# Kernel tuning notes

Measured on AMD Instinct MI355X. Metric: run time of the kernel, lower is better.

## Reference

```python
import jax, jax.numpy as jnp
import numpy as np
import math

B, S, D, H, HD = 2, 2048, 2048, 16, 128
ROPE_THETA = 10000.0


def _rope_cache(seq_len, dim, base, dtype=jnp.float32):
    inv_freq = 1.0 / (base ** (jnp.arange(0, dim, 2, dtype=jnp.float32) / dim))
    t = jnp.arange(seq_len, dtype=jnp.float32)
    freqs = jnp.einsum('i,j->ij', t, inv_freq)          # [S, dim/2]
    emb = jnp.concatenate([freqs, freqs], axis=-1)       # [S, dim]
    return jnp.cos(emb).astype(dtype), jnp.sin(emb).astype(dtype)


def _rotate_half(x):
    x1, x2 = x[..., : x.shape[-1] // 2], x[..., x.shape[-1] // 2:]
    return jnp.concatenate([-x2, x1], axis=-1)


def setup_inputs() -> dict:
    key = jax.random.key(0)
    ks = jax.random.split(key, 6)
    hidden_states = jax.random.normal(ks[0], (B, S, D), dtype=jnp.float32) * 0.02
    w_scale = 1.0 / math.sqrt(D)
    Wq = jax.random.normal(ks[1], (D, D), dtype=jnp.float32) * w_scale
    Wk = jax.random.normal(ks[2], (D, D), dtype=jnp.float32) * w_scale
    Wv = jax.random.normal(ks[3], (D, D), dtype=jnp.float32) * w_scale
    Wo = jax.random.normal(ks[4], (D, D), dtype=jnp.float32) * w_scale
    # additive causal mask [B, 1, S, S]: 0 on/below diag, large negative above
    causal = jnp.tril(jnp.ones((S, S), dtype=bool))
    attention_mask = jnp.where(causal, 0.0, -1e9).astype(jnp.float32)
    attention_mask = jnp.broadcast_to(attention_mask[None, None], (B, 1, S, S))
    position_ids = jnp.broadcast_to(jnp.arange(S, dtype=jnp.int32)[None], (B, S))
    return {
        'hidden_states': hidden_states,
        'attention_mask': attention_mask,
        'position_ids': position_ids,
        'Wq': Wq, 'Wk': Wk, 'Wv': Wv, 'Wo': Wo,
    }


def reference(hidden_states, attention_mask, position_ids, Wq, Wk, Wv, Wo):
    bsz, q_len, _ = hidden_states.shape
    # projections (torch Linear: x @ W.T), then split heads -> [B, H, S, HD]
    def proj(W):
        return jnp.einsum('bsd,ed->bse', hidden_states, W).reshape(bsz, q_len, H, HD).transpose(0, 2, 1, 3)
    q, k, v = proj(Wq), proj(Wk), proj(Wv)
    cos_c, sin_c = _rope_cache(q_len, HD, ROPE_THETA, hidden_states.dtype)
    cos = cos_c[position_ids][:, None]  # [B, 1, S, HD]
    sin = sin_c[position_ids][:, None]
    q = q * cos + _rotate_half(q) * sin
    k = k * cos + _rotate_half(k) * sin
    scores = jnp.einsum('bhqd,bhkd->bhqk', q, k) / math.sqrt(HD)
    scores = scores + attention_mask
    attn_weights = jax.nn.softmax(scores.astype(jnp.float32), axis=-1).astype(q.dtype)
    attn_out = jnp.einsum('bhqk,bhkd->bhqd', attn_weights, v)
    attn_out = attn_out.transpose(0, 2, 1, 3).reshape(bsz, q_len, D)
    out = jnp.einsum('bsd,ed->bse', attn_out, Wo)
    return out
```

## Files before the change

kernel.cpp:

```cpp
#include <hip/hip_runtime.h>

typedef __bf16 bf16;
typedef __bf16 bf16x8 __attribute__((ext_vector_type(8)));
typedef float f32x4 __attribute__((ext_vector_type(4)));

#define D_MODEL 2048
#define SEQ 2048
#define NH 16
#define HEAD_DIM 128
#define NBATCH 2
#define SM_SCALE 0.08838834764831845f
#define WSEG 4194304
#define NT_TILES 32

typedef __attribute__((address_space(1))) const void* gas_cp;
typedef __attribute__((address_space(3))) void* las_p;
__device__ __forceinline__ void ll16(const bf16* g, bf16* l) {
  __builtin_amdgcn_global_load_lds((gas_cp)g, (las_p)l, 16, 0, 0);
}

__device__ __forceinline__ bf16x8 cvt8(const float* p) {
  float4 a = *(const float4*)p;
  float4 b = *(const float4*)(p + 4);
  bf16x8 v;
  v[0] = (bf16)a.x; v[1] = (bf16)a.y; v[2] = (bf16)a.z; v[3] = (bf16)a.w;
  v[4] = (bf16)b.x; v[5] = (bf16)b.y; v[6] = (bf16)b.z; v[7] = (bf16)b.w;
  return v;
}

__global__ __launch_bounds__(256)
void cvt_hidden(const float* __restrict__ src, bf16* __restrict__ dst) {
  size_t i = ((size_t)blockIdx.x * 256 + threadIdx.x) * 8;
  *(bf16x8*)(dst + i) = cvt8(src + i);
}

__global__ __launch_bounds__(256)
void cvt_weights(const float* __restrict__ w0, const float* __restrict__ w1,
                 const float* __restrict__ w2, const float* __restrict__ w3,
                 bf16* __restrict__ dst) {
  const float* src = (blockIdx.y == 0) ? w0 : (blockIdx.y == 1) ? w1
                   : (blockIdx.y == 2) ? w2 : w3;
  size_t i = ((size_t)blockIdx.x * 256 + threadIdx.x) * 8;
  *(bf16x8*)(dst + (size_t)blockIdx.y * WSEG + i) = cvt8(src + i);
}

#define LDF256(DA, DB, SB, KX)                                               \
  _Pragma("unroll") for (int mi = 0; mi < 8; mi++)                           \
      DA[mi] = *(const bf16x8*)((SB) + ((arowQ + mi * 16) << 7) + (KX));     \
  DB[0] = *(const bf16x8*)((SB) + 32768 + (qb0 << 7) + (KX));                \
  DB[1] = *(const bf16x8*)((SB) + 32768 + (qb1 << 7) + (KX));                \
  DB[2] = *(const bf16x8*)((SB) + 32768 + (qb2 << 7) + (KX));                \
  DB[3] = *(const bf16x8*)((SB) + 32768 + (qb3 << 7) + (KX));

#define MM256(AF, BF)                                                        \
  _Pragma("unroll") for (int mi = 0; mi < 8; mi++)                           \
  _Pragma("unroll") for (int ni = 0; ni < 4; ni++)                           \
      acc[mi][ni] = __builtin_amdgcn_mfma_f32_16x16x32_bf16(                 \
          AF[mi], BF[ni], acc[mi][ni], 0, 0, 0);

#define ST2(GP, ROW0, KT, LB)                                                \
  ll16((GP) + (size_t)((ROW0) + w * 8 + l8) * D_MODEL + (KT) * 64 + kelem,   \
       (bf16*)((LB) + w * 1024));

__global__ __launch_bounds__(512, 2)
void gemm256(const bf16* __restrict__ A, const bf16* __restrict__ W,
             bf16* __restrict__ Qo, bf16* __restrict__ Ko,
             bf16* __restrict__ Vo, const int* __restrict__ pos_ids) {
  __shared__ __align__(16) char smem[131072];

  const int tid  = threadIdx.x;
  const int lane = tid & 63;
  const int w    = tid >> 6;
  const int quad = lane >> 4, l15 = lane & 15;
  const int l8   = lane >> 3, l7 = lane & 7;
  const int kelem = 8 * (l7 ^ l8);
  const int wm2 = w >> 2;
  const int wn2 = w & 3;
  const int hh  = wn2 >> 1;
  const int cb  = (wn2 & 1) * 32;

  const int bid = blockIdx.x;
  const int lin = (bid & 7) * 48 + (bid >> 3);
  const int by = lin / 24, bx = lin % 24;
  const int mBase = by << 8, nBase = bx << 8;

  const int kx0 = (quad * 16) ^ ((l15 & 7) << 4);
  const int kx1 = kx0 ^ 64;
  const int arowQ = wm2 * 128 + l15;
  const int qb0 = hh * 128 + cb + l15;
  const int qb1 = qb0 + 16, qb2 = qb0 + 64, qb3 = qb0 + 80;

  f32x4 acc[8][4];
#pragma unroll
  for (int i = 0; i < 8; i++)
#pragma unroll
    for (int j = 0; j < 4; j++) acc[i][j] = 0.0f;

  bf16x8 aP[8], bP[4];
  bf16x8 aQ[8], bQ[4];

  {
    char* s0 = smem;
    ST2(A, mBase,       0, s0 + 0);
    ST2(A, mBase + 64,  0, s0 + 8192);
    ST2(A, mBase + 128, 0, s0 + 16384);
    ST2(A, mBase + 192, 0, s0 + 24576);
    ST2(W, nBase,       0, s0 + 32768);
    ST2(W, nBase + 64,  0, s0 + 40960);
    ST2(W, nBase + 128, 0, s0 + 49152);
    ST2(W, nBase + 192, 0, s0 + 57344);
  }
  asm volatile("s_waitcnt vmcnt(0)" ::: "memory");
  __builtin_amdgcn_s_barrier();
  LDF256(aP, bP, smem, kx0);

  int buf = 0;
  for (int t = 0; t < NT_TILES; ++t) {
    char* const Sb = smem + buf * 65536;
    char* const Ob = smem + (buf ^ 1) * 65536;
    const bool pf  = (t + 1 < NT_TILES);

    LDF256(aQ, bQ, Sb, kx1);
    if (pf) {
      ST2(A, mBase,       t + 1, Ob + 0);
      ST2(A, mBase + 64,  t + 1, Ob + 8192);
      ST2(A, mBase + 128, t + 1, Ob + 16384);
      ST2(A, mBase + 192, t + 1, Ob + 24576);
      ST2(W, nBase,       t + 1, Ob + 32768);
      ST2(W, nBase + 64,  t + 1, Ob + 40960);
      ST2(W, nBase + 128, t + 1, Ob + 49152);
      ST2(W, nBase + 192, t + 1, Ob + 57344);
    }
    __builtin_amdgcn_sched_barrier(0);
    __builtin_amdgcn_s_setprio(1);
    MM256(aP, bP);
    __builtin_amdgcn_s_setprio(0);
    asm volatile("s_waitcnt lgkmcnt(0)" ::: "memory");
    asm volatile("s_waitcnt vmcnt(0)" ::: "memory");
    __builtin_amdgcn_s_barrier();

    if (pf) {
      LDF256(aP, bP, Ob, kx0);
    }
    __builtin_amdgcn_sched_barrier(0);
    __builtin_amdgcn_s_setprio(1);
    MM256(aQ, bQ);
    __builtin_amdgcn_s_setprio(0);
    asm volatile("s_waitcnt lgkmcnt(0)" ::: "memory");

    buf ^= 1;
  }

  const int matrix = nBase >> 11;
  const int nb     = nBase & 2047;
  if (matrix == 2) {
    const int h = (nb >> 7) + hh;
#pragma unroll
    for (int mi = 0; mi < 8; mi++)
#pragma unroll
      for (int ni = 0; ni < 4; ni++) {
        const int hd = cb + (ni & 1) * 16 + (ni >> 1) * 64 + l15;
#pragma unroll
        for (int r = 0; r < 4; r++) {
          int m = mBase + wm2 * 128 + mi * 16 + quad * 4 + r;
          int b = m >> 11, s2 = m & 2047;
          Vo[((size_t)((b * NH + h) * HEAD_DIM + hd)) * SEQ + s2] =
              (bf16)acc[mi][ni][r];
        }
      }
  } else {
    bf16* Out = (matrix == 0) ? Qo : Ko;
    float invf[2];
#pragma unroll
    for (int ni = 0; ni < 2; ni++)
      invf[ni] = __expf(-(float)(cb + ni * 16 + l15) *
                        (9.210340371976184f / 64.0f));
#pragma unroll
    for (int mi = 0; mi < 8; mi++)
#pragma unroll
      for (int r = 0; r < 4; r++) {
        int m = mBase + wm2 * 128 + mi * 16 + quad * 4 + r;
        float pos = (float)pos_ids[m];
        bf16* op = Out + (size_t)m * D_MODEL + nb + hh * 128 + cb + l15;
#pragma unroll
        for (int ni = 0; ni < 2; ni++) {
          float sn, cs;
          __sincosf(pos * invf[ni], &sn, &cs);
          float q0 = acc[mi][ni][r];
          float q1 = acc[mi][ni + 2][r];
          op[ni * 16]      = (bf16)(q0 * cs - q1 * sn);
          op[ni * 16 + 64] = (bf16)(q1 * cs + q0 * sn);
        }
      }
  }
}

#define LDFRAG(DA, DB, SB, KX)                                               \
  _Pragma("unroll") for (int mi = 0; mi < 4; mi++)                           \
      DA[mi] = *(const bf16x8*)((SB) + ((arow + mi * 16) << 7) + (KX));      \
  DB[0] = *(const bf16x8*)((SB) + 16384 + (rb0 << 7) + (KX));                \
  DB[1] = *(const bf16x8*)((SB) + 16384 + (rb1 << 7) + (KX));                \
  DB[2] = *(const bf16x8*)((SB) + 16384 + (rb2 << 7) + (KX));                \
  DB[3] = *(const bf16x8*)((SB) + 16384 + (rb3 << 7) + (KX));

#define MMAC(AF, BF)                                                         \
  _Pragma("unroll") for (int mi = 0; mi < 4; mi++)                           \
  _Pragma("unroll") for (int ni = 0; ni < 4; ni++)                           \
      acc[mi][ni] = __builtin_amdgcn_mfma_f32_16x16x32_bf16(                 \
          AF[mi], BF[ni], acc[mi][ni], 0, 0, 0);

#define ST1(GP, ROW0, KT, LB)                                                \
  ll16((GP) + (size_t)((ROW0) + w * 8 + l8) * D_MODEL + (KT) * 64 + kelem,   \
       (bf16*)((LB) + w * 1024));

__global__ __launch_bounds__(512, 2)
void gemm_proj(const bf16* __restrict__ A, const bf16* __restrict__ W,
               float* __restrict__ C) {
  __shared__ __align__(16) char smem[147456];

  const int tid  = threadIdx.x;
  const int lane = tid & 63;
  const int w    = tid >> 6;
  const int quad = lane >> 4, l15 = lane & 15;
  const int l8   = lane >> 3, l7 = lane & 7;
  const int kelem = 8 * (l7 ^ l8);
  const int wm = w >> 2;
  const int wn = w & 3;

  const int bid = blockIdx.x;
  const int lin = (bid & 7) * 32 + (bid >> 3);
  const int by = lin >> 3, bx = lin & 7;
  const int mBase = by << 7, nBase = bx << 8;

  const int kx0 = (quad * 16) ^ ((l15 & 7) << 4);
  const int kx1 = kx0 ^ 64;
  const int arow = wm * 64 + l15;
  const int rb0 = wn * 64 + l15;
  const int rb1 = rb0 + 16, rb2 = rb0 + 32, rb3 = rb0 + 48;

  f32x4 acc[4][4];
#pragma unroll
  for (int i = 0; i < 4; i++)
#pragma unroll
    for (int j = 0; j < 4; j++) acc[i][j] = 0.0f;

  bf16x8 aP[4], bP[4], aQ[4], bQ[4];

  {
    char* s0 = smem;
    char* s1 = smem + 49152;
    ST1(A, mBase,       0, s0 + 0);
    ST1(A, mBase + 64,  0, s0 + 8192);
    ST1(W, nBase,       0, s0 + 16384);
    ST1(W, nBase + 64,  0, s0 + 24576);
    ST1(W, nBase + 128, 0, s0 + 32768);
    ST1(W, nBase + 192, 0, s0 + 40960);
    ST1(A, mBase,       1, s1 + 0);
    ST1(A, mBase + 64,  1, s1 + 8192);
    ST1(W, nBase,       1, s1 + 16384);
    ST1(W, nBase + 64,  1, s1 + 24576);
    ST1(W, nBase + 128, 1, s1 + 32768);
    ST1(W, nBase + 192, 1, s1 + 40960);
  }
  asm volatile("s_waitcnt vmcnt(6)" ::: "memory");
  __builtin_amdgcn_s_barrier();
  LDFRAG(aP, bP, smem, kx0);

  int buf = 0;
  for (int t = 0; t < NT_TILES; ++t) {
    char* const Sb  = smem + buf * 49152;
    const int  nb1  = (buf + 1 == 3) ? 0 : buf + 1;
    const int  pb   = (buf + 2 >= 3) ? buf - 1 : buf + 2;
    char* const Nb  = smem + nb1 * 49152;
    char* const Pb  = smem + pb * 49152;
    const bool pf   = (t + 2 < NT_TILES);

    LDFRAG(aQ, bQ, Sb, kx1);
    if (pf) {
      ST1(A, mBase,      t + 2, Pb + 0);
      ST1(A, mBase + 64, t + 2, Pb + 8192);
      ST1(W, nBase,      t + 2, Pb + 16384);
    }
    __builtin_amdgcn_sched_barrier(0);
    __builtin_amdgcn_s_setprio(1);
    MMAC(aP, bP);
    __builtin_amdgcn_s_setprio(0);
    asm volatile("s_waitcnt lgkmcnt(0)" ::: "memory");
    if (pf)
      asm volatile("s_waitcnt vmcnt(3)" ::: "memory");
    else
      asm volatile("s_waitcnt vmcnt(0)" ::: "memory");
    __builtin_amdgcn_s_barrier();

    if (t + 1 < NT_TILES) {
      LDFRAG(aP, bP, Nb, kx0);
    }
    if (pf) {
      ST1(W, nBase + 64,  t + 2, Pb + 24576);
      ST1(W, nBase + 128, t + 2, Pb + 32768);
      ST1(W, nBase + 192, t + 2, Pb + 40960);
    }
    __builtin_amdgcn_sched_barrier(0);
    __builtin_amdgcn_s_setprio(1);
    MMAC(aQ, bQ);
    __builtin_amdgcn_s_setprio(0);
    asm volatile("s_waitcnt lgkmcnt(0)" ::: "memory");
    __builtin_amdgcn_s_barrier();

    buf = nb1;
  }

#pragma unroll
  for (int mi = 0; mi < 4; mi++) {
    const int m = mBase + wm * 64 + mi * 16 + quad * 4;
#pragma unroll
    for (int ni = 0; ni < 4; ni++) {
      const int n = nBase + wn * 64 + ni * 16 + l15;
      float* cp = C + (size_t)m * D_MODEL + n;
#pragma unroll
      for (int r = 0; r < 4; r++) cp[(size_t)r * D_MODEL] = acc[mi][ni][r];
    }
  }
}

__global__ __launch_bounds__(256, 3)
void attn_mfma(const bf16* __restrict__ Q, const bf16* __restrict__ K,
               const bf16* __restrict__ Vt, bf16* __restrict__ O) {
  __shared__ __align__(16) bf16 K_lds[64 * 136];
  __shared__ __align__(16) bf16 V_lds[128 * 72];
  __shared__ __align__(16) bf16 P_lds[64 * 72];

  const int tid  = threadIdx.x;
  const int lane = tid & 63;
  const int w    = tid >> 6;
  const int quad = lane >> 4, l15 = lane & 15;
  const int s    = 31 - blockIdx.y;
  const int bh   = blockIdx.x;
  const size_t qkBase = (size_t)(bh >> 4) * SEQ * D_MODEL + (size_t)(bh & 15) * HEAD_DIM;
  const size_t vBase  = (size_t)bh * HEAD_DIM * SEQ;

  const int qbase = s * 64 + w * 16;

  bf16x8 qa[4];
#pragma unroll
  for (int kk = 0; kk < 4; kk++)
    qa[kk] = *(const bf16x8*)(Q + qkBase + (size_t)(qbase + l15) * D_MODEL + kk * 32 + quad * 8);

  bf16x8 ones;
#pragma unroll
  for (int i = 0; i < 8; i++) ones[i] = (bf16)1.0f;

  f32x4 oacc[8], ls;
#pragma unroll
  for (int ni = 0; ni < 8; ni++) oacc[ni] = 0.0f;
  ls = 0.0f;

  const int ntiles = s + 1;

  bf16x8 kr[4], vr[4];
  auto loadKV = [&](int t0) {
#pragma unroll
    for (int i = 0; i < 4; i++) {
      int c = tid + 256 * i;
      kr[i] = *(const bf16x8*)(K + qkBase + (size_t)(t0 + (c >> 4)) * D_MODEL + (c & 15) * 8);
    }
#pragma unroll
    for (int i = 0; i < 4; i++) {
      int c = tid + 256 * i;
      vr[i] = *(const bf16x8*)(Vt + vBase + (size_t)(c >> 3) * SEQ + t0 + (c & 7) * 8);
    }
  };
  loadKV(0);

  const int prow = w * 16;

  for (int tt = 0; tt < ntiles; tt++) {
    const int t0 = tt * 64;
    __syncthreads();
#pragma unroll
    for (int i = 0; i < 4; i++) {
      int c = tid + 256 * i;
      *(bf16x8*)&K_lds[(c >> 4) * 136 + (c & 15) * 8] = kr[i];
    }
#pragma unroll
    for (int i = 0; i < 4; i++) {
      int c = tid + 256 * i;
      *(bf16x8*)&V_lds[(c >> 3) * 72 + (c & 7) * 8] = vr[i];
    }
    __syncthreads();
    if (tt + 1 < ntiles) loadKV(t0 + 64);

    f32x4 sacc[4];
#pragma unroll
    for (int ni = 0; ni < 4; ni++) sacc[ni] = 0.0f;
#pragma unroll
    for (int kk = 0; kk < 4; kk++) {
#pragma unroll
      for (int ni = 0; ni < 4; ni++) {
        bf16x8 kf = *(const bf16x8*)&K_lds[(ni * 16 + l15) * 136 + kk * 32 + quad * 8];
        sacc[ni] = __builtin_amdgcn_mfma_f32_16x16x32_bf16(qa[kk], kf, sacc[ni], 0, 0, 0);
      }
    }

    if (tt == s) {
#pragma unroll
      for (int r = 0; r < 4; r++) {
        int qrow = qbase + quad * 4 + r;
#pragma unroll
        for (int ni = 0; ni < 4; ni++) {
          int tcol = t0 + ni * 16 + l15;
          float pv = (tcol <= qrow) ? __expf(fminf(sacc[ni][r] * SM_SCALE, 30.0f)) : 0.0f;
          P_lds[(prow + quad * 4 + r) * 72 + ni * 16 + l15] = (bf16)pv;
        }
      }
    } else {
#pragma unroll
      for (int r = 0; r < 4; r++)
#pragma unroll
        for (int ni = 0; ni < 4; ni++)
          P_lds[(prow + quad * 4 + r) * 72 + ni * 16 + l15] =
              (bf16)__expf(fminf(sacc[ni][r] * SM_SCALE, 30.0f));
    }

#pragma unroll
    for (int kk2 = 0; kk2 < 2; kk2++) {
      bf16x8 pf = *(const bf16x8*)&P_lds[(prow + l15) * 72 + kk2 * 32 + quad * 8];
#pragma unroll
      for (int ni = 0; ni < 8; ni++) {
        bf16x8 vf = *(const bf16x8*)&V_lds[(ni * 16 + l15) * 72 + kk2 * 32 + quad * 8];
        oacc[ni] = __builtin_amdgcn_mfma_f32_16x16x32_bf16(pf, vf, oacc[ni], 0, 0, 0);
      }
      ls = __builtin_amdgcn_mfma_f32_16x16x32_bf16(pf, ones, ls, 0, 0, 0);
    }
  }

#pragma unroll
  for (int r = 0; r < 4; r++) {
    float inv = 1.0f / ls[r];
    bf16* op = O + qkBase + (size_t)(qbase + quad * 4 + r) * D_MODEL;
#pragma unroll
    for (int ni = 0; ni < 8; ni++)
      op[ni * 16 + l15] = (bf16)(oacc[ni][r] * inv);
  }
}

extern "C" void kernel_launch(void* const* d_in, const int* in_sizes, int n_in,
                              void* d_out, int out_size, void* d_ws, size_t ws_size,
                              hipStream_t stream) {
  const float* hidden = (const float*)d_in[0];
  const int* pos = (const int*)d_in[2];
  const float* Wq = (const float*)d_in[3];
  const float* Wk = (const float*)d_in[4];
  const float* Wv = (const float*)d_in[5];
  const float* Wo = (const float*)d_in[6];
  float* out = (float*)d_out;

  const size_t TENS = (size_t)NBATCH * SEQ * D_MODEL;
  bf16* Qb = (bf16*)d_ws;
  bf16* Kb = Qb + TENS;
  bf16* Vt = Kb + TENS;
  bf16* AO = Vt + TENS;
  bf16* Hb = AO + TENS;
  bf16* Wb = Hb + TENS;

  cvt_hidden<<<dim3(TENS / 2048), dim3(256), 0, stream>>>(hidden, Hb);
  cvt_weights<<<dim3(WSEG / 2048, 4), dim3(256), 0, stream>>>(Wq, Wk, Wv, Wo, Wb);

  gemm256<<<dim3(384), dim3(512), 0, stream>>>(Hb, Wb, Qb, Kb, Vt, pos);

  attn_mfma<<<dim3(NBATCH * NH, 32), dim3(256), 0, stream>>>(Qb, Kb, Vt, AO);

  gemm_proj<<<dim3(256), dim3(512), 0, stream>>>(
      AO, Wb + 3 * (size_t)WSEG, out);
}
```

Baseline: 370.4 us.

## Rewrite attention with 128-row Q blocks, async LDS double-buffered KV, swizzled layout

The attention kernel now processes 128 query rows per block with 8 waves, so each K/V tile loaded into LDS is reused by twice as many queries. K/V tiles are copied straight into double-buffered LDS with global_load_lds instead of passing through registers, and an XOR swizzle replaces row padding to avoid bank conflicts. Waves whose rows lie entirely before the current key tile skip the tile's compute, which keeps the causal work balanced. In exchange there is a full vmcnt wait and barrier every tile, and fewer blocks with more LDS per block, which lowers occupancy.

```diff
diff --git a/kernel.cpp b/kernel.cpp
--- a/kernel.cpp
+++ b/kernel.cpp
@@ -323,28 +323,31 @@
   }
 }
 
-__global__ __launch_bounds__(256, 3)
-void attn_mfma(const bf16* __restrict__ Q, const bf16* __restrict__ K,
-               const bf16* __restrict__ Vt, bf16* __restrict__ O) {
-  __shared__ __align__(16) bf16 K_lds[64 * 136];
-  __shared__ __align__(16) bf16 V_lds[128 * 72];
-  __shared__ __align__(16) bf16 P_lds[64 * 72];
+__global__ __launch_bounds__(512, 2)
+void attn_v2(const bf16* __restrict__ Q, const bf16* __restrict__ K,
+             const bf16* __restrict__ Vt, bf16* __restrict__ O) {
+  __shared__ __align__(16) bf16 Kl[2][64 * 128];
+  __shared__ __align__(16) bf16 Vl[2][128 * 64];
+  __shared__ __align__(16) bf16 P_lds[128 * 72];
 
   const int tid  = threadIdx.x;
   const int lane = tid & 63;
   const int w    = tid >> 6;
   const int quad = lane >> 4, l15 = lane & 15;
-  const int s    = 31 - blockIdx.y;
+  const int l8   = lane >> 3, l7 = lane & 7;
+  const int qi   = 15 - (int)blockIdx.y;
   const int bh   = blockIdx.x;
   const size_t qkBase = (size_t)(bh >> 4) * SEQ * D_MODEL + (size_t)(bh & 15) * HEAD_DIM;
   const size_t vBase  = (size_t)bh * HEAD_DIM * SEQ;
 
-  const int qbase = s * 64 + w * 16;
+  const int qbw  = qi * 128 + w * 16;
+  const int prow = w * 16;
+  const int kswz = (l15 & 7) << 3;
 
   bf16x8 qa[4];
 #pragma unroll
   for (int kk = 0; kk < 4; kk++)
-    qa[kk] = *(const bf16x8*)(Q + qkBase + (size_t)(qbase + l15) * D_MODEL + kk * 32 + quad * 8);
+    qa[kk] = *(const bf16x8*)(Q + qkBase + (size_t)(qbw + l15) * D_MODEL + kk * 32 + quad * 8);
 
   bf16x8 ones;
 #pragma unroll
@@ -355,89 +358,87 @@
   for (int ni = 0; ni < 8; ni++) oacc[ni] = 0.0f;
   ls = 0.0f;
 
-  const int ntiles = s + 1;
-
-  bf16x8 kr[4], vr[4];
-  auto loadKV = [&](int t0) {
-#pragma unroll
-    for (int i = 0; i < 4; i++) {
-      int c = tid + 256 * i;
-      kr[i] = *(const bf16x8*)(K + qkBase + (size_t)(t0 + (c >> 4)) * D_MODEL + (c & 15) * 8);
-    }
-#pragma unroll
-    for (int i = 0; i < 4; i++) {
-      int c = tid + 256 * i;
-      vr[i] = *(const bf16x8*)(Vt + vBase + (size_t)(c >> 3) * SEQ + t0 + (c & 7) * 8);
-    }
-  };
-  loadKV(0);
-
-  const int prow = w * 16;
-
-  for (int tt = 0; tt < ntiles; tt++) {
+  const int nt = 2 * qi + 2;
+
+#define STAGE_KV(T0, BUF)                                                    \
+  _Pragma("unroll") for (int i_ = 0; i_ < 2; i_++) {                         \
+    const int u_ = w * 2 + i_;                                               \
+    const int rK = u_ * 4 + quad;                                            \
+    ll16(K + qkBase + (size_t)((T0) + rK) * D_MODEL + 8 * (l15 ^ (rK & 7)),  \
+         &Kl[BUF][u_ * 512]);                                                \
+    const int rV = u_ * 8 + l8;                                              \
+    ll16(Vt + vBase + (size_t)rV * SEQ + (T0) + 8 * (l7 ^ (rV & 7)),         \
+         &Vl[BUF][u_ * 512]);                                                \
+  }
+
+  STAGE_KV(0, 0);
+  asm volatile("s_waitcnt vmcnt(0)" ::: "memory");
+  __builtin_amdgcn_s_barrier();
+
+  int cur = 0;
+  for (int tt = 0; tt < nt; ++tt, cur ^= 1) {
     const int t0 = tt * 64;
-    __syncthreads();
-#pragma unroll
-    for (int i = 0; i < 4; i++) {
-      int c = tid + 256 * i;
-      *(bf16x8*)&K_lds[(c >> 4) * 136 + (c & 15) * 8] = kr[i];
-    }
-#pragma unroll
-    for (int i = 0; i < 4; i++) {
-      int c = tid + 256 * i;
-      *(bf16x8*)&V_lds[(c >> 3) * 72 + (c & 7) * 8] = vr[i];
-    }
-    __syncthreads();
-    if (tt + 1 < ntiles) loadKV(t0 + 64);
-
-    f32x4 sacc[4];
-#pragma unroll
-    for (int ni = 0; ni < 4; ni++) sacc[ni] = 0.0f;
-#pragma unroll
-    for (int kk = 0; kk < 4; kk++) {
-#pragma unroll
-      for (int ni = 0; ni < 4; ni++) {
-        bf16x8 kf = *(const bf16x8*)&K_lds[(ni * 16 + l15) * 136 + kk * 32 + quad * 8];
-        sacc[ni] = __builtin_amdgcn_mfma_f32_16x16x32_bf16(qa[kk], kf, sacc[ni], 0, 0, 0);
-      }
-    }
-
-    if (tt == s) {
-#pragma unroll
-      for (int r = 0; r < 4; r++) {
-        int qrow = qbase + quad * 4 + r;
+    if (tt + 1 < nt) STAGE_KV(t0 + 64, cur ^ 1);
+
+    if (t0 <= qbw + 15) {
+      const bf16* Kc = &Kl[cur][0];
+      const bf16* Vc = &Vl[cur][0];
+
+      f32x4 sacc[4];
+#pragma unroll
+      for (int ni = 0; ni < 4; ni++) sacc[ni] = 0.0f;
+#pragma unroll
+      for (int kk = 0; kk < 4; kk++) {
 #pragma unroll
         for (int ni = 0; ni < 4; ni++) {
-          int tcol = t0 + ni * 16 + l15;
-          float pv = (tcol <= qrow) ? __expf(fminf(sacc[ni][r] * SM_SCALE, 30.0f)) : 0.0f;
-          P_lds[(prow + quad * 4 + r) * 72 + ni * 16 + l15] = (bf16)pv;
+          bf16x8 kf = *(const bf16x8*)&Kc[(ni * 16 + l15) * 128 +
+                                          (((kk * 32 + quad * 8)) ^ kswz)];
+          sacc[ni] = __builtin_amdgcn_mfma_f32_16x16x32_bf16(qa[kk], kf, sacc[ni], 0, 0, 0);
         }
       }
-    } else {
-#pragma unroll
-      for (int r = 0; r < 4; r++)
-#pragma unroll
-        for (int ni = 0; ni < 4; ni++)
-          P_lds[(prow + quad * 4 + r) * 72 + ni * 16 + l15] =
-              (bf16)__expf(fminf(sacc[ni][r] * SM_SCALE, 30.0f));
-    }
-
-#pragma unroll
-    for (int kk2 = 0; kk2 < 2; kk2++) {
-      bf16x8 pf = *(const bf16x8*)&P_lds[(prow + l15) * 72 + kk2 * 32 + quad * 8];
-#pragma unroll
-      for (int ni = 0; ni < 8; ni++) {
-        bf16x8 vf = *(const bf16x8*)&V_lds[(ni * 16 + l15) * 72 + kk2 * 32 + quad * 8];
-        oacc[ni] = __builtin_amdgcn_mfma_f32_16x16x32_bf16(pf, vf, oacc[ni], 0, 0, 0);
+
+      if (t0 + 63 > qbw) {
+#pragma unroll
+        for (int r = 0; r < 4; r++) {
+          int qrow = qbw + quad * 4 + r;
+#pragma unroll
+          for (int ni = 0; ni < 4; ni++) {
+            int tcol = t0 + ni * 16 + l15;
+            float pv = (tcol <= qrow) ? __expf(fminf(sacc[ni][r] * SM_SCALE, 30.0f)) : 0.0f;
+            P_lds[(prow + quad * 4 + r) * 72 + ni * 16 + l15] = (bf16)pv;
+          }
+        }
+      } else {
+#pragma unroll
+        for (int r = 0; r < 4; r++)
+#pragma unroll
+          for (int ni = 0; ni < 4; ni++)
+            P_lds[(prow + quad * 4 + r) * 72 + ni * 16 + l15] =
+                (bf16)__expf(fminf(sacc[ni][r] * SM_SCALE, 30.0f));
       }
-      ls = __builtin_amdgcn_mfma_f32_16x16x32_bf16(pf, ones, ls, 0, 0, 0);
-    }
-  }
+
+#pragma unroll
+      for (int kk2 = 0; kk2 < 2; kk2++) {
+        bf16x8 pf = *(const bf16x8*)&P_lds[(prow + l15) * 72 + kk2 * 32 + quad * 8];
+#pragma unroll
+        for (int ni = 0; ni < 8; ni++) {
+          bf16x8 vf = *(const bf16x8*)&Vc[(ni * 16 + l15) * 64 +
+                                          (((kk2 * 32 + quad * 8)) ^ kswz)];
+          oacc[ni] = __builtin_amdgcn_mfma_f32_16x16x32_bf16(pf, vf, oacc[ni], 0, 0, 0);
+        }
+        ls = __builtin_amdgcn_mfma_f32_16x16x32_bf16(pf, ones, ls, 0, 0, 0);
+      }
+    }
+
+    asm volatile("s_waitcnt vmcnt(0)" ::: "memory");
+    __builtin_amdgcn_s_barrier();
+  }
+#undef STAGE_KV
 
 #pragma unroll
   for (int r = 0; r < 4; r++) {
     float inv = 1.0f / ls[r];
-    bf16* op = O + qkBase + (size_t)(qbase + quad * 4 + r) * D_MODEL;
+    bf16* op = O + qkBase + (size_t)(qbw + quad * 4 + r) * D_MODEL;
 #pragma unroll
     for (int ni = 0; ni < 8; ni++)
       op[ni * 16 + l15] = (bf16)(oacc[ni][r] * inv);
@@ -468,7 +469,7 @@
 
   gemm256<<<dim3(384), dim3(512), 0, stream>>>(Hb, Wb, Qb, Kb, Vt, pos);
 
-  attn_mfma<<<dim3(NBATCH * NH, 32), dim3(256), 0, stream>>>(Qb, Kb, Vt, AO);
+  attn_v2<<<dim3(NBATCH * NH, 16), dim3(512), 0, stream>>>(Qb, Kb, Vt, AO);
 
   gemm_proj<<<dim3(256), dim3(512), 0, stream>>>(
       AO, Wb + 3 * (size_t)WSEG, out);
```

Result: no change. 364.3 us (-1.7%).
